# Kernel optimization log

Measured on AMD Instinct MI355X. Metric: run time of the kernel, lower is better.

## Reference

```python
import jax, jax.numpy as jnp
import numpy as np

K = 1024            # atoms per chain
L = 4 * K - 9       # 2*(K-3) sin/cos dihedrals + (K-2) len13 + (K-1) bond lengths
EPS = 1e-6


def _denorm(v, lo, hi):
    # map [-1, 1] -> [lo, hi]
    return (v + 1.0) * 0.5 * (hi - lo) + lo


def _output_arr2values(v):
    # split flat NN output into (sin/cos dihedrals, hedron len13, bond lengths)
    n_d = K - 3
    sc = v[: 2 * n_d].reshape(n_d, 2)                     # (sin, cos) per dihedral
    d13 = _denorm(v[2 * n_d : 2 * n_d + K - 2], 1.5, 5.0)  # 1-3 distances, [1.5, 5]
    bl = _denorm(v[2 * n_d + K - 2 :], 0.9, 3.0)           # bond lengths,  [0.9, 3]
    return sc, d13, bl


def _len2ang(sc, d13, bl):
    # bond angles via law of cosines from consecutive bond lengths + 1-3 distance
    l1, l2 = bl[:-1], bl[1:]
    ct = (l1 * l1 + l2 * l2 - d13 * d13) / (2.0 * l1 * l2)
    theta = jnp.arccos(jnp.clip(ct, -1.0 + EPS, 1.0 - EPS))   # (K-2,) radians
    chi = jnp.arctan2(sc[:, 0], sc[:, 1])                      # (K-3,) radians
    return theta, chi


def _len_ang2coords(bl, theta, chi):
    # sequential NeRF chain extension: place atom i from atoms i-3, i-2, i-1
    a0 = jnp.zeros(3, dtype=bl.dtype)
    a1 = jnp.array([1.0, 0.0, 0.0], dtype=bl.dtype) * bl[0]
    t0 = theta[0]
    a2 = a1 + bl[1] * jnp.stack([-jnp.cos(t0), jnp.sin(t0), jnp.zeros((), bl.dtype)])

    def step(carry, inp):
        a, b, c = carry
        l, th, ch = inp
        bc = c - b
        bc = bc / (jnp.linalg.norm(bc) + EPS)
        n = jnp.cross(b - a, bc)
        n = n / (jnp.linalg.norm(n) + EPS)
        m = jnp.cross(n, bc)
        st = jnp.sin(th)
        d = c + l * (-jnp.cos(th) * bc + st * jnp.cos(ch) * m + st * jnp.sin(ch) * n)
        return (b, c, d), d

    _, rest = jax.lax.scan(step, (a0, a1, a2), (bl[2:], theta[1:], chi))
    return jnp.concatenate([jnp.stack([a0, a1, a2]), rest], axis=0)  # (K, 3)


def _chain2coords(v):
    sc, d13, bl = _output_arr2values(v)
    theta, chi = _len2ang(sc, d13, bl)
    return _len_ang2coords(bl, theta, chi)


def setup_inputs() -> dict:
    key = jax.random.key(0)
    k1, k2 = jax.random.split(key)
    B = 2048
    predictions = 2.0 * jax.random.uniform(k1, (B, L), dtype=jnp.float32) - 1.0
    targets = 2.0 * jax.random.uniform(k2, (B, L), dtype=jnp.float32) - 1.0
    return {"predictions": predictions, "targets": targets}


def reference(predictions, targets):
    p = jnp.clip(predictions, -1.0, 1.0)           # only predictions are clamped
    pred_coords = jax.vmap(_chain2coords)(p)        # (B, K, 3)
    targ_coords = jax.vmap(_chain2coords)(targets)  # (B, K, 3)
    return jnp.mean(jnp.square(pred_coords - targ_coords))
```

## Files before the change

kernel.cpp:

```cpp
#include <hip/hip_runtime.h>


#define LROW  4087
#define NSTEP 1021
#define NROW  2048
#define CHUNK 16
#define EPSF  1e-6f
#define INVMEAN (1.0f / (2048.0f * 1024.0f * 3.0f))

__device__ __forceinline__ float frcp(float x){ return __builtin_amdgcn_rcpf(x); }
__device__ __forceinline__ float frsq(float x){ return __builtin_amdgcn_rsqf(x); }

__global__ void __launch_bounds__(128) __attribute__((amdgpu_waves_per_eu(4, 4)))
rmsd_kernel(const float* __restrict__ pred, const float* __restrict__ targ,
            float* __restrict__ ws){
  __shared__ float pos[64*49 + 48 + 2];
  __shared__ float ini[3];

  const int row  = blockIdx.x;
  const int tid  = threadIdx.x;
  const int ln   = tid & 63;
  const int wv   = tid >> 6;
  const int j0   = ln * CHUNK;

  const float* __restrict__ v = (wv ? targ : pred) + (size_t)row * LROW;
  const float cl = wv ? 1e30f : 1.0f;

  const float rb0 = fminf(fmaxf(v[3064], -cl), cl);
  const float rd0 = fminf(fmaxf(v[2042], -cl), cl);
  const float rb1w= fminf(fmaxf(v[3065], -cl), cl);

  float s0[CHUNK], s1[CHUNK], dd[CHUNK], bv[CHUNK+1];
  #pragma unroll
  for (int k = 0; k < CHUNK; ++k){
    s0[k] = v[2*(j0+k)];
    s1[k] = v[2*(j0+k)+1];
    dd[k] = v[2043 + j0 + k];
  }
  #pragma unroll
  for (int m = 0; m <= CHUNK; ++m){
    int ix = 3065 + j0 + m;
    if (ix > 4086) ix = 4086;
    bv[m] = v[ix];
  }
  #pragma unroll
  for (int m = 0; m <= CHUNK; ++m)
    bv[m] = fmaf(fminf(fmaxf(bv[m], -cl), cl), 1.05f, 1.95f);

  float c0x,c0y,c0z, c1x,c1y,c1z, c2x,c2y,c2z, tx,ty,tz;
  float tl[CHUNK][3];
  #pragma unroll
  for (int k = 0; k < CHUNK; ++k){
    const float a0 = fminf(fmaxf(s0[k], -cl), cl);
    const float a1 = fminf(fmaxf(s1[k], -cl), cl);
    const float d  = fmaf(fminf(fmaxf(dd[k], -cl), cl), 1.75f, 3.25f);
    const float b1 = bv[k], b2 = bv[k+1];
    float ct = (b1*b1 + b2*b2 - d*d) * frcp(2.0f*b1*b2);
    ct = fminf(fmaxf(ct, -1.0f + EPSF), 1.0f - EPSF);
    const float omc = fmaxf(1.0f - ct*ct, 1e-12f);
    const float ist = frsq(omc);
    const float st  = omc * ist;
    const float r2 = a0*a0 + a1*a1;
    const bool ok = r2 > 1e-36f;
    const float ir = ok ? frsq(r2) : 0.0f;
    const float scv = a0 * ir;
    const float ccv = ok ? a1 * ir : 1.0f;
    const float hx = -ct, hy = st*ccv, hz = st*scv;
    if (k == 0){
      c0x=hx;      c0y=hy;      c0z=hz;
      c1x=-st;     c1y=hx*ccv;  c1z=hx*scv;
      c2x=0.0f;    c2y=-scv;    c2z=ccv;
      tx=b2*hx;    ty=b2*hy;    tz=b2*hz;
    } else {
      const float n0x = c0x*hx + c1x*hy + c2x*hz;
      const float n0y = c0y*hx + c1y*hy + c2y*hz;
      const float n0z = c0z*hx + c1z*hy + c2z*hz;
      tx = fmaf(b2, n0x, tx); ty = fmaf(b2, n0y, ty); tz = fmaf(b2, n0z, tz);
      const float n1x = ist * fmaf(hx, n0x, -c0x);
      const float n1y = ist * fmaf(hx, n0y, -c0y);
      const float n1z = ist * fmaf(hx, n0z, -c0z);
      const float n2x = fmaf(ccv, c2x, -scv*c1x);
      const float n2y = fmaf(ccv, c2y, -scv*c1y);
      const float n2z = fmaf(ccv, c2z, -scv*c1z);
      c0x=n0x; c0y=n0y; c0z=n0z;
      c1x=n1x; c1y=n1y; c1z=n1z;
      c2x=n2x; c2y=n2y; c2z=n2z;
    }
    tl[k][0]=tx; tl[k][1]=ty; tl[k][2]=tz;
  }

  float r0x=c0x, r0y=c0y, r0z=c0z, r1x=c1x, r1y=c1y, r1z=c1z;
  #pragma unroll
  for (int off = 1; off < 64; off <<= 1){
    const float o0x=__shfl_up(r0x,off), o0y=__shfl_up(r0y,off), o0z=__shfl_up(r0z,off);
    const float o1x=__shfl_up(r1x,off), o1y=__shfl_up(r1y,off), o1z=__shfl_up(r1z,off);
    const float o2x = o0y*o1z - o0z*o1y;
    const float o2y = o0z*o1x - o0x*o1z;
    const float o2z = o0x*o1y - o0y*o1x;
    const float n0x = o0x*r0x + o1x*r0y + o2x*r0z;
    const float n0y = o0y*r0x + o1y*r0y + o2y*r0z;
    const float n0z = o0z*r0x + o1z*r0y + o2z*r0z;
    const float n1x = o0x*r1x + o1x*r1y + o2x*r1z;
    const float n1y = o0y*r1x + o1y*r1y + o2y*r1z;
    const float n1z = o0z*r1x + o1z*r1y + o2z*r1z;
    if (ln >= off){
      r0x=n0x; r0y=n0y; r0z=n0z;
      r1x=n1x; r1y=n1y; r1z=n1z;
    }
  }

  float e0x=__shfl_up(r0x,1), e0y=__shfl_up(r0y,1), e0z=__shfl_up(r0z,1);
  float e1x=__shfl_up(r1x,1), e1y=__shfl_up(r1y,1), e1z=__shfl_up(r1z,1);
  if (ln == 0){ e0x=1.f; e0y=0.f; e0z=0.f; e1x=0.f; e1y=1.f; e1z=0.f; }

  {
    const float x2x = e0y*e1z - e0z*e1y;
    const float x2y = e0z*e1x - e0x*e1z;
    const float x2z = e0x*e1y - e0y*e1x;
    const float wx = e0x*tx + e1x*ty + x2x*tz;
    const float wy = e0y*tx + e1y*ty + x2y*tz;
    const float wz = e0z*tx + e1z*ty + x2z*tz;
    float sx=wx, sy=wy, sz=wz;
    #pragma unroll
    for (int off = 1; off < 64; off <<= 1){
      const float ax=__shfl_up(sx,off), ay=__shfl_up(sy,off), az=__shfl_up(sz,off);
      if (ln >= off){ sx+=ax; sy+=ay; sz+=az; }
    }
    tx = sx - wx; ty = sy - wy; tz = sz - wz;
  }

  const float bl0 = fmaf(rb0,  1.05f, 1.95f);
  const float d0  = fmaf(rd0,  1.75f, 3.25f);
  const float b1f = fmaf(rb1w, 1.05f, 1.95f);
  float ct0 = (bl0*bl0 + b1f*b1f - d0*d0) * frcp(2.0f*bl0*b1f);
  ct0 = fminf(fmaxf(ct0, -1.0f + EPSF), 1.0f - EPSF);
  const float st0 = sqrtf(fmaxf(1.0f - ct0*ct0, 0.0f));
  const float a1x = bl0;
  const float a2x = bl0 - b1f*ct0;
  const float a2y = b1f*st0;

  const float e2x = e0y*e1z - e0z*e1y;
  const float e2y = e0z*e1x - e0x*e1z;
  const float e2z = e0x*e1y - e0y*e1x;

  const float g0x = -ct0*e0x - st0*e0y, g0y = st0*e0x - ct0*e0y, g0z = e0z;
  const float g1x = -ct0*e1x - st0*e1y, g1y = st0*e1x - ct0*e1y, g1z = e1z;
  const float g2x = -ct0*e2x - st0*e2y, g2y = st0*e2x - ct0*e2y, g2z = e2z;
  const float gtx = a2x - ct0*tx - st0*ty;
  const float gty = a2y + st0*tx - ct0*ty;
  const float gtz = tz;

  #pragma unroll
  for (int k = 0; k < CHUNK; ++k){
    const float ux = tl[k][0], uy = tl[k][1], uz = tl[k][2];
    tl[k][0] = gtx + g0x*ux + g1x*uy + g2x*uz;
    tl[k][1] = gty + g0y*ux + g1y*uy + g2y*uz;
    tl[k][2] = gtz + g0z*ux + g1z*uy + g2z*uz;
  }

  if (wv == 0){
    #pragma unroll
    for (int k = 0; k < CHUNK; ++k){
      if (j0 + k < NSTEP){
        const int o = ln*49 + 3*k;
        pos[o] = tl[k][0]; pos[o+1] = tl[k][1]; pos[o+2] = tl[k][2];
      }
    }
    if (ln == 0){ ini[0] = a1x; ini[1] = a2x; ini[2] = a2y; }
  }
  __syncthreads();

  if (wv == 1){
    float acc = 0.0f;
    if (ln == 0){
      const float dx = ini[0] - a1x;
      const float dy = ini[1] - a2x;
      const float dz = ini[2] - a2y;
      acc = dx*dx + dy*dy + dz*dz;
    }
    #pragma unroll
    for (int k = 0; k < CHUNK; ++k){
      if (j0 + k < NSTEP){
        const int o = ln*49 + 3*k;
        const float dx = pos[o]   - tl[k][0];
        const float dy = pos[o+1] - tl[k][1];
        const float dz = pos[o+2] - tl[k][2];
        acc = fmaf(dx, dx, acc);
        acc = fmaf(dy, dy, acc);
        acc = fmaf(dz, dz, acc);
      }
    }
    #pragma unroll
    for (int off = 32; off > 0; off >>= 1) acc += __shfl_down(acc, off);
    if (ln == 0) ws[row] = acc;
  }
}

__global__ void __launch_bounds__(256, 1)
reduce_kernel(const float* __restrict__ ws, float* __restrict__ out){
  __shared__ float wsum[4];
  const int tid = threadIdx.x;
  float a = 0.0f;
  #pragma unroll
  for (int i = 0; i < 8; ++i) a += ws[tid + (i << 8)];
  #pragma unroll
  for (int off = 32; off > 0; off >>= 1) a += __shfl_down(a, off);
  if ((tid & 63) == 0) wsum[tid >> 6] = a;
  __syncthreads();
  if (tid == 0) out[0] = (wsum[0] + wsum[1] + wsum[2] + wsum[3]) * INVMEAN;
}

extern "C" void kernel_launch(void* const* d_in, const int* in_sizes, int n_in,
                              void* d_out, int out_size, void* d_ws, size_t ws_size,
                              hipStream_t stream) {
  const float* pred = (const float*)d_in[0];
  const float* targ = (const float*)d_in[1];
  float* out = (float*)d_out;
  float* ws  = (float*)d_ws;

  rmsd_kernel<<<NROW, 128, 0, stream>>>(pred, targ, ws);
  reduce_kernel<<<1, 256, 0, stream>>>(ws, out);
}
```

Before: 96.73 us.

## Process pred and target chains in one wave and fold relative transform

Each block is now a single 64-lane wave that runs the chain scan for both the prediction and the target row, replacing the two-wave design that exchanged positions through shared memory and a barrier. The error is computed in the prediction's local frame: the combined rotation P^T·T and offset are formed once per lane, then applied to the target's local positions, which avoids transforming both chains to global coordinates. The shared-memory staging and the sync go away. In exchange each wave holds two sets of 48 tail registers and does serial work for two chains, with occupancy forced down to 2 waves per EU, so latency hiding may suffer.

```diff
diff --git a/kernel.cpp b/kernel.cpp
--- a/kernel.cpp
+++ b/kernel.cpp
@@ -11,24 +11,22 @@
 __device__ __forceinline__ float frcp(float x){ return __builtin_amdgcn_rcpf(x); }
 __device__ __forceinline__ float frsq(float x){ return __builtin_amdgcn_rsqf(x); }
 
-__global__ void __launch_bounds__(128) __attribute__((amdgpu_waves_per_eu(4, 4)))
-rmsd_kernel(const float* __restrict__ pred, const float* __restrict__ targ,
-            float* __restrict__ ws){
-  __shared__ float pos[64*49 + 48 + 2];
-  __shared__ float ini[3];
-
-  const int row  = blockIdx.x;
-  const int tid  = threadIdx.x;
-  const int ln   = tid & 63;
-  const int wv   = tid >> 6;
-  const int j0   = ln * CHUNK;
-
-  const float* __restrict__ v = (wv ? targ : pred) + (size_t)row * LROW;
-  const float cl = wv ? 1e30f : 1.0f;
-
-  const float rb0 = fminf(fmaxf(v[3064], -cl), cl);
-  const float rd0 = fminf(fmaxf(v[2042], -cl), cl);
-  const float rb1w= fminf(fmaxf(v[3065], -cl), cl);
+template<bool CLIP>
+__device__ __forceinline__ void chainScan(
+    const float* __restrict__ v, const int ln, const int j0,
+    float tl[CHUNK][3],
+    float &g0x, float &g0y, float &g0z,
+    float &g1x, float &g1y, float &g1z,
+    float &g2x, float &g2y, float &g2z,
+    float &gtx, float &gty, float &gtz,
+    float &a1x, float &a2x, float &a2y)
+{
+  float rb0 = v[3064], rd0 = v[2042], rb1 = v[3065];
+  if (CLIP){
+    rb0 = fminf(fmaxf(rb0, -1.f), 1.f);
+    rd0 = fminf(fmaxf(rd0, -1.f), 1.f);
+    rb1 = fminf(fmaxf(rb1, -1.f), 1.f);
+  }
 
   float s0[CHUNK], s1[CHUNK], dd[CHUNK], bv[CHUNK+1];
   #pragma unroll
@@ -41,30 +39,32 @@
   for (int m = 0; m <= CHUNK; ++m){
     int ix = 3065 + j0 + m;
     if (ix > 4086) ix = 4086;
-    bv[m] = v[ix];
-  }
-  #pragma unroll
-  for (int m = 0; m <= CHUNK; ++m)
-    bv[m] = fmaf(fminf(fmaxf(bv[m], -cl), cl), 1.05f, 1.95f);
+    float b = v[ix];
+    if (CLIP) b = fminf(fmaxf(b, -1.f), 1.f);
+    bv[m] = fmaf(b, 1.05f, 1.95f);
+  }
 
   float c0x,c0y,c0z, c1x,c1y,c1z, c2x,c2y,c2z, tx,ty,tz;
-  float tl[CHUNK][3];
   #pragma unroll
   for (int k = 0; k < CHUNK; ++k){
-    const float a0 = fminf(fmaxf(s0[k], -cl), cl);
-    const float a1 = fminf(fmaxf(s1[k], -cl), cl);
-    const float d  = fmaf(fminf(fmaxf(dd[k], -cl), cl), 1.75f, 3.25f);
+    float a0 = s0[k], a1v = s1[k], dr = dd[k];
+    if (CLIP){
+      a0  = fminf(fmaxf(a0,  -1.f), 1.f);
+      a1v = fminf(fmaxf(a1v, -1.f), 1.f);
+      dr  = fminf(fmaxf(dr,  -1.f), 1.f);
+    }
+    const float d  = fmaf(dr, 1.75f, 3.25f);
     const float b1 = bv[k], b2 = bv[k+1];
     float ct = (b1*b1 + b2*b2 - d*d) * frcp(2.0f*b1*b2);
     ct = fminf(fmaxf(ct, -1.0f + EPSF), 1.0f - EPSF);
     const float omc = fmaxf(1.0f - ct*ct, 1e-12f);
     const float ist = frsq(omc);
     const float st  = omc * ist;
-    const float r2 = a0*a0 + a1*a1;
+    const float r2 = a0*a0 + a1v*a1v;
     const bool ok = r2 > 1e-36f;
     const float ir = ok ? frsq(r2) : 0.0f;
     const float scv = a0 * ir;
-    const float ccv = ok ? a1 * ir : 1.0f;
+    const float ccv = ok ? a1v * ir : 1.0f;
     const float hx = -ct, hy = st*ccv, hz = st*scv;
     if (k == 0){
       c0x=hx;      c0y=hy;      c0z=hz;
@@ -129,71 +129,86 @@
     tx = sx - wx; ty = sy - wy; tz = sz - wz;
   }
 
-  const float bl0 = fmaf(rb0,  1.05f, 1.95f);
-  const float d0  = fmaf(rd0,  1.75f, 3.25f);
-  const float b1f = fmaf(rb1w, 1.05f, 1.95f);
+  const float bl0 = fmaf(rb0, 1.05f, 1.95f);
+  const float d0  = fmaf(rd0, 1.75f, 3.25f);
+  const float b1f = fmaf(rb1, 1.05f, 1.95f);
   float ct0 = (bl0*bl0 + b1f*b1f - d0*d0) * frcp(2.0f*bl0*b1f);
   ct0 = fminf(fmaxf(ct0, -1.0f + EPSF), 1.0f - EPSF);
   const float st0 = sqrtf(fmaxf(1.0f - ct0*ct0, 0.0f));
-  const float a1x = bl0;
-  const float a2x = bl0 - b1f*ct0;
-  const float a2y = b1f*st0;
+  a1x = bl0;
+  a2x = bl0 - b1f*ct0;
+  a2y = b1f*st0;
 
   const float e2x = e0y*e1z - e0z*e1y;
   const float e2y = e0z*e1x - e0x*e1z;
   const float e2z = e0x*e1y - e0y*e1x;
 
-  const float g0x = -ct0*e0x - st0*e0y, g0y = st0*e0x - ct0*e0y, g0z = e0z;
-  const float g1x = -ct0*e1x - st0*e1y, g1y = st0*e1x - ct0*e1y, g1z = e1z;
-  const float g2x = -ct0*e2x - st0*e2y, g2y = st0*e2x - ct0*e2y, g2z = e2z;
-  const float gtx = a2x - ct0*tx - st0*ty;
-  const float gty = a2y + st0*tx - ct0*ty;
-  const float gtz = tz;
-
+  g0x = -ct0*e0x - st0*e0y; g0y = st0*e0x - ct0*e0y; g0z = e0z;
+  g1x = -ct0*e1x - st0*e1y; g1y = st0*e1x - ct0*e1y; g1z = e1z;
+  g2x = -ct0*e2x - st0*e2y; g2y = st0*e2x - ct0*e2y; g2z = e2z;
+  gtx = a2x - ct0*tx - st0*ty;
+  gty = a2y + st0*tx - ct0*ty;
+  gtz = tz;
+}
+
+__global__ void __launch_bounds__(64) __attribute__((amdgpu_waves_per_eu(2, 2)))
+rmsd_kernel(const float* __restrict__ pred, const float* __restrict__ targ,
+            float* __restrict__ ws){
+  const int row = blockIdx.x;
+  const int ln  = threadIdx.x;
+  const int j0  = ln * CHUNK;
+
+  const float* __restrict__ vp = pred + (size_t)row * LROW;
+  const float* __restrict__ vt = targ + (size_t)row * LROW;
+
+  float tlP[CHUNK][3], tlT[CHUNK][3];
+  float P0x,P0y,P0z, P1x,P1y,P1z, P2x,P2y,P2z, Ptx,Pty,Ptz, Pa1,Pa2x,Pa2y;
+  float T0x,T0y,T0z, T1x,T1y,T1z, T2x,T2y,T2z, Ttx,Tty,Ttz, Ta1,Ta2x,Ta2y;
+
+  chainScan<true >(vp, ln, j0, tlP, P0x,P0y,P0z, P1x,P1y,P1z, P2x,P2y,P2z,
+                   Ptx,Pty,Ptz, Pa1,Pa2x,Pa2y);
+  chainScan<false>(vt, ln, j0, tlT, T0x,T0y,T0z, T1x,T1y,T1z, T2x,T2y,T2z,
+                   Ttx,Tty,Ttz, Ta1,Ta2x,Ta2y);
+
+  const float D00 = P0x*T0x + P0y*T0y + P0z*T0z;
+  const float D10 = P1x*T0x + P1y*T0y + P1z*T0z;
+  const float D20 = P2x*T0x + P2y*T0y + P2z*T0z;
+  const float D01 = P0x*T1x + P0y*T1y + P0z*T1z;
+  const float D11 = P1x*T1x + P1y*T1y + P1z*T1z;
+  const float D21 = P2x*T1x + P2y*T1y + P2z*T1z;
+  const float D02 = P0x*T2x + P0y*T2y + P0z*T2z;
+  const float D12 = P1x*T2x + P1y*T2y + P1z*T2z;
+  const float D22 = P2x*T2x + P2y*T2y + P2z*T2z;
+  const float bx = Ttx - Ptx, by = Tty - Pty, bz = Ttz - Ptz;
+  const float dtx = P0x*bx + P0y*by + P0z*bz;
+  const float dty = P1x*bx + P1y*by + P1z*bz;
+  const float dtz = P2x*bx + P2y*by + P2z*bz;
+
+  float acc = 0.0f;
+  if (ln == 0){
+    const float dx = Pa1  - Ta1;
+    const float dy = Pa2x - Ta2x;
+    const float dz = Pa2y - Ta2y;
+    acc = dx*dx + dy*dy + dz*dz;
+  }
   #pragma unroll
   for (int k = 0; k < CHUNK; ++k){
-    const float ux = tl[k][0], uy = tl[k][1], uz = tl[k][2];
-    tl[k][0] = gtx + g0x*ux + g1x*uy + g2x*uz;
-    tl[k][1] = gty + g0y*ux + g1y*uy + g2y*uz;
-    tl[k][2] = gtz + g0z*ux + g1z*uy + g2z*uz;
-  }
-
-  if (wv == 0){
-    #pragma unroll
-    for (int k = 0; k < CHUNK; ++k){
-      if (j0 + k < NSTEP){
-        const int o = ln*49 + 3*k;
-        pos[o] = tl[k][0]; pos[o+1] = tl[k][1]; pos[o+2] = tl[k][2];
-      }
-    }
-    if (ln == 0){ ini[0] = a1x; ini[1] = a2x; ini[2] = a2y; }
-  }
-  __syncthreads();
-
-  if (wv == 1){
-    float acc = 0.0f;
-    if (ln == 0){
-      const float dx = ini[0] - a1x;
-      const float dy = ini[1] - a2x;
-      const float dz = ini[2] - a2y;
-      acc = dx*dx + dy*dy + dz*dz;
-    }
-    #pragma unroll
-    for (int k = 0; k < CHUNK; ++k){
-      if (j0 + k < NSTEP){
-        const int o = ln*49 + 3*k;
-        const float dx = pos[o]   - tl[k][0];
-        const float dy = pos[o+1] - tl[k][1];
-        const float dz = pos[o+2] - tl[k][2];
-        acc = fmaf(dx, dx, acc);
-        acc = fmaf(dy, dy, acc);
-        acc = fmaf(dz, dz, acc);
-      }
-    }
-    #pragma unroll
-    for (int off = 32; off > 0; off >>= 1) acc += __shfl_down(acc, off);
-    if (ln == 0) ws[row] = acc;
-  }
+    if (j0 + k < NSTEP){
+      const float vx = tlT[k][0], vy = tlT[k][1], vz = tlT[k][2];
+      const float wx = dtx + D00*vx + D01*vy + D02*vz;
+      const float wy = dty + D10*vx + D11*vy + D12*vz;
+      const float wz = dtz + D20*vx + D21*vy + D22*vz;
+      const float dx = tlP[k][0] - wx;
+      const float dy = tlP[k][1] - wy;
+      const float dz = tlP[k][2] - wz;
+      acc = fmaf(dx, dx, acc);
+      acc = fmaf(dy, dy, acc);
+      acc = fmaf(dz, dz, acc);
+    }
+  }
+  #pragma unroll
+  for (int off = 32; off > 0; off >>= 1) acc += __shfl_down(acc, off);
+  if (ln == 0) ws[row] = acc;
 }
 
 __global__ void __launch_bounds__(256, 1)
@@ -218,6 +233,6 @@
   float* out = (float*)d_out;
   float* ws  = (float*)d_ws;
 
-  rmsd_kernel<<<NROW, 128, 0, stream>>>(pred, targ, ws);
+  rmsd_kernel<<<NROW, 64, 0, stream>>>(pred, targ, ws);
   reduce_kernel<<<1, 256, 0, stream>>>(ws, out);
 }
```

Measured after the change: 101.1 us. +4.5%, slower.
